# Kernel optimization log

Measured on AMD Instinct MI355X. Metric: run time of the kernel, lower is better.

## Reference

```python
import jax, jax.numpy as jnp
import numpy as np

B, S, D = 2, 4096, 1024
H, W = 16, 128
HD = D // H  # 64


def setup_inputs() -> dict:
    key = jax.random.key(0)
    ks = jax.random.split(key, 6)
    x = jax.random.normal(ks[0], (B, S, D), dtype=jnp.float32)
    # standard RoPE angle table: theta[pos, i] = pos / 10000^(2i/hd)
    inv_freq = 1.0 / (10000.0 ** (jnp.arange(0, HD, 2, dtype=jnp.float32) / HD))  # (hd/2,)
    rope_freqs = jnp.arange(S, dtype=jnp.float32)[:, None] * inv_freq[None, :]     # (S, hd/2)
    scale = 0.02
    wq = jax.random.normal(ks[1], (D, D), dtype=jnp.float32) * scale
    wk = jax.random.normal(ks[2], (D, D), dtype=jnp.float32) * scale
    wv = jax.random.normal(ks[3], (D, D), dtype=jnp.float32) * scale
    wo = jax.random.normal(ks[4], (D, D), dtype=jnp.float32) * scale
    return {"x": x, "rope_freqs": rope_freqs, "wq": wq, "wk": wk, "wv": wv, "wo": wo}


def reference(x, rope_freqs, wq, wk, wv, wo):
    Bsz, Sl, Dm = x.shape
    hd = Dm // H
    q = (x @ wq.T).reshape(Bsz, Sl, H, hd)
    k = (x @ wk.T).reshape(Bsz, Sl, H, hd)
    v = (x @ wv.T).reshape(Bsz, Sl, H, hd)

    # rotate-half RoPE, angles broadcast over batch and heads
    f = rope_freqs[:Sl]                               # (S, hd/2)
    cos = jnp.cos(f)[None, :, None, :]
    sin = jnp.sin(f)[None, :, None, :]

    def rope(t):
        t1, t2 = jnp.split(t, 2, axis=-1)
        return jnp.concatenate([t1 * cos - t2 * sin, t2 * cos + t1 * sin], axis=-1)

    q = rope(q)
    k = rope(k)

    # block-local sliding-window attention: window [q-left, q+right]
    Bk = W                       # block size == window size
    nb = Sl // Bk                # S assumed divisible by W
    left = W // 2
    right = W - left - 1

    pad = [(0, 0), (Bk, Bk), (0, 0), (0, 0)]
    kb = jnp.pad(k, pad).reshape(Bsz, nb + 2, Bk, H, hd)
    vb = jnp.pad(v, pad).reshape(Bsz, nb + 2, Bk, H, hd)
    # each query block attends to 3 consecutive key blocks (prev, self, next)
    k3 = jnp.concatenate([kb[:, :-2], kb[:, 1:-1], kb[:, 2:]], axis=2)  # (B,nb,3Bk,H,hd)
    v3 = jnp.concatenate([vb[:, :-2], vb[:, 1:-1], vb[:, 2:]], axis=2)
    qb = q.reshape(Bsz, nb, Bk, H, hd)

    scale = 1.0 / jnp.sqrt(jnp.asarray(hd, dtype=x.dtype))
    scores = jnp.einsum('bnqhd,bnkhd->bnhqk', qb, k3) * scale  # (B,nb,H,Bk,3Bk)

    r = jnp.arange(Bk)
    c = jnp.arange(3 * Bk)
    rel = c[None, :] - Bk - r[:, None]                  # key_pos - query_pos, (Bk,3Bk)
    win = (rel >= -left) & (rel <= right)
    blk = jnp.arange(nb)
    key_pos = blk[:, None] * Bk + c[None, :] - Bk       # (nb,3Bk) absolute key positions
    valid = (key_pos >= 0) & (key_pos < Sl)
    mask = win[None, :, :] & valid[:, None, :]          # (nb,Bk,3Bk)

    scores = jnp.where(mask[None, :, None, :, :], scores, jnp.asarray(-1e30, scores.dtype))
    probs = jax.nn.softmax(scores, axis=-1)
    out = jnp.einsum('bnhqk,bnkhd->bnqhd', probs, v3).reshape(Bsz, Sl, H * hd)
    return out @ wo.T
```

## Files before the change

### kernel.cpp

```cpp
#include <hip/hip_runtime.h>

typedef unsigned short u16;
typedef unsigned int   u32;
typedef __attribute__((ext_vector_type(4))) unsigned int u32x4;
typedef __attribute__((ext_vector_type(2))) unsigned int u32x2;
typedef __attribute__((ext_vector_type(8))) short        s16x8;
typedef __attribute__((ext_vector_type(4))) float        f32x4;
typedef __attribute__((ext_vector_type(2))) float        f32x2;

#define S_LEN 4096

typedef const __attribute__((address_space(1))) void gas_void;
typedef __attribute__((address_space(3))) void las_void;

__device__ __forceinline__ u16 f2bf(float f) {
    u32 u = __builtin_bit_cast(u32, f);
    u32 r = (u + 0x7fffu + ((u >> 16) & 1u)) >> 16;
    return (u16)r;
}

__device__ __forceinline__ float rmax16(float v) {
    v = fmaxf(v, __shfl_xor(v, 1));
    v = fmaxf(v, __shfl_xor(v, 2));
    v = fmaxf(v, __shfl_xor(v, 4));
    v = fmaxf(v, __shfl_xor(v, 8));
    return v;
}
__device__ __forceinline__ float rsum16(float v) {
    v += __shfl_xor(v, 1);
    v += __shfl_xor(v, 2);
    v += __shfl_xor(v, 4);
    v += __shfl_xor(v, 8);
    return v;
}

__global__ __launch_bounds__(256)
void prep_kernel(const float* __restrict__ x,
                 const float* __restrict__ wq, const float* __restrict__ wk,
                 const float* __restrict__ wv, const float* __restrict__ wo,
                 const float* __restrict__ freqs,
                 u16* __restrict__ xb, u16* __restrict__ wqkv, u16* __restrict__ wob,
                 float* __restrict__ tab) {
    const int bid = blockIdx.x;
    const int t   = threadIdx.x;
    if (bid < 8192) {
        const int i = bid * 256 + t;
        const f32x4 v = *(const f32x4*)(x + (size_t)i * 4);
        u32x2 o;
        o.x = (u32)f2bf(v.x) | ((u32)f2bf(v.y) << 16);
        o.y = (u32)f2bf(v.z) | ((u32)f2bf(v.w) << 16);
        *(u32x2*)(xb + (size_t)i * 4) = o;
    } else if (bid < 12288) {
        const int i   = (bid - 8192) * 256 + t;
        const int sel = i >> 18;
        const int loc = i & 262143;
        const float* src = (sel == 0) ? wq : (sel == 1) ? wk : (sel == 2) ? wv : wo;
        u16* dst = (sel < 3) ? (wqkv + (size_t)sel * 1048576) : wob;
        const f32x4 v = *(const f32x4*)(src + (size_t)loc * 4);
        u32x2 o;
        o.x = (u32)f2bf(v.x) | ((u32)f2bf(v.y) << 16);
        o.y = (u32)f2bf(v.z) | ((u32)f2bf(v.w) << 16);
        *(u32x2*)(dst + (size_t)loc * 4) = o;
    } else {
        const int i = (bid - 12288) * 256 + t;
        const float f = freqs[i];
        float sn, cs;
        sincosf(f, &sn, &cs);
        tab[i * 2]     = cs;
        tab[i * 2 + 1] = sn;
    }
}

#define VMW0() asm volatile("s_waitcnt vmcnt(0)" ::: "memory")
#define LGKM0() do { asm volatile("s_waitcnt lgkmcnt(0)" ::: "memory"); \
                     __builtin_amdgcn_sched_barrier(0); } while (0)
#define DSR0(d, a)   asm volatile("ds_read_b128 %0, %1"              : "=v"(d) : "v"(a))
#define DSR(d, a, o) asm volatile("ds_read_b128 %0, %1 offset:" #o   : "=v"(d) : "v"(a))
#define MFMA16(a, b, c) __builtin_amdgcn_mfma_f32_16x16x32_bf16(a, b, c, 0, 0, 0)
#define GL(p, d) __builtin_amdgcn_global_load_lds((gas_void*)(p), (las_void*)(d), 16, 0, 0)

#define FRAGS(P) s16x8 P##a0,P##a1,P##a2,P##a3,P##a4,P##a5,P##a6,P##a7, \
                       P##b0,P##b1,P##b2,P##b3,P##b4,P##b5,P##b6,P##b7

#define LOADTILE(P, CUR) do { \
    const u32 abase_ = ldsA + ((u32)(CUR) << 14) + arow; \
    const u32 bbase_ = ldsB + ((u32)(CUR) << 15) + brow; \
    const u32 aa0_ = abase_ + ck0, aa1_ = abase_ + ck1; \
    const u32 ba0_ = bbase_ + ck0, ba1_ = bbase_ + ck1; \
    DSR0(P##a0, aa0_); DSR(P##a1, aa0_, 2048); DSR(P##a2, aa0_, 4096); DSR(P##a3, aa0_, 6144); \
    DSR0(P##a4, aa1_); DSR(P##a5, aa1_, 2048); DSR(P##a6, aa1_, 4096); DSR(P##a7, aa1_, 6144); \
    DSR0(P##b0, ba0_); DSR(P##b1, ba0_, 2048); DSR(P##b2, ba0_, 4096); DSR(P##b3, ba0_, 6144); \
    DSR0(P##b4, ba1_); DSR(P##b5, ba1_, 2048); DSR(P##b6, ba1_, 4096); DSR(P##b7, ba1_, 6144); \
} while (0)

#define MFMA32(P) do { \
    __builtin_amdgcn_s_setprio(1); \
    acc[0][0]=MFMA16(P##a0,P##b0,acc[0][0]); acc[1][0]=MFMA16(P##a1,P##b0,acc[1][0]); \
    acc[2][0]=MFMA16(P##a2,P##b0,acc[2][0]); acc[3][0]=MFMA16(P##a3,P##b0,acc[3][0]); \
    acc[0][1]=MFMA16(P##a0,P##b1,acc[0][1]); acc[1][1]=MFMA16(P##a1,P##b1,acc[1][1]); \
    acc[2][1]=MFMA16(P##a2,P##b1,acc[2][1]); acc[3][1]=MFMA16(P##a3,P##b1,acc[3][1]); \
    acc[0][2]=MFMA16(P##a0,P##b2,acc[0][2]); acc[1][2]=MFMA16(P##a1,P##b2,acc[1][2]); \
    acc[2][2]=MFMA16(P##a2,P##b2,acc[2][2]); acc[3][2]=MFMA16(P##a3,P##b2,acc[3][2]); \
    acc[0][3]=MFMA16(P##a0,P##b3,acc[0][3]); acc[1][3]=MFMA16(P##a1,P##b3,acc[1][3]); \
    acc[2][3]=MFMA16(P##a2,P##b3,acc[2][3]); acc[3][3]=MFMA16(P##a3,P##b3,acc[3][3]); \
    acc[0][0]=MFMA16(P##a4,P##b4,acc[0][0]); acc[1][0]=MFMA16(P##a5,P##b4,acc[1][0]); \
    acc[2][0]=MFMA16(P##a6,P##b4,acc[2][0]); acc[3][0]=MFMA16(P##a7,P##b4,acc[3][0]); \
    acc[0][1]=MFMA16(P##a4,P##b5,acc[0][1]); acc[1][1]=MFMA16(P##a5,P##b5,acc[1][1]); \
    acc[2][1]=MFMA16(P##a6,P##b5,acc[2][1]); acc[3][1]=MFMA16(P##a7,P##b5,acc[3][1]); \
    acc[0][2]=MFMA16(P##a4,P##b6,acc[0][2]); acc[1][2]=MFMA16(P##a5,P##b6,acc[1][2]); \
    acc[2][2]=MFMA16(P##a6,P##b6,acc[2][2]); acc[3][2]=MFMA16(P##a7,P##b6,acc[3][2]); \
    acc[0][3]=MFMA16(P##a4,P##b7,acc[0][3]); acc[1][3]=MFMA16(P##a5,P##b7,acc[1][3]); \
    acc[2][3]=MFMA16(P##a6,P##b7,acc[2][3]); acc[3][3]=MFMA16(P##a7,P##b7,acc[3][3]); \
    __builtin_amdgcn_s_setprio(0); \
} while (0)

template<int MODE>
__global__ __launch_bounds__(512, 2)
void gemm_bt(const u16* __restrict__ A, const u16* __restrict__ Bw,
             void* __restrict__ Cv, const float* __restrict__ cstab) {
    __shared__ __align__(16) u16 As[2][8192];
    __shared__ __align__(16) u16 Bs[2][16384];
    const int t    = threadIdx.x;
    const int bm   = blockIdx.x << 7;
    const int bn   = blockIdx.y << 8;
    const int wave = t >> 6;
    const int wr   = (wave >> 2) & 1;
    const int wc   = wave & 3;
    const int lane = t & 63;
    const int fr   = lane & 15;
    const int kg   = lane >> 4;
    const int f7   = fr & 7;
    const int wq16 = wave << 9;
    const int K    = 1024;

    const int srow = t >> 3;
    const int cSw  = (t & 7) ^ (srow & 7);

    const u16* ga0 = A  + (size_t)(bm + srow) * K + (cSw << 3);
    const u16* ga1 = ga0 + (size_t)64 * K;
    const u16* gb0 = Bw + (size_t)(bn + srow) * K + (cSw << 3);
    const u16* gb1 = gb0 + (size_t)64 * K;
    const u16* gb2 = gb1 + (size_t)64 * K;
    const u16* gb3 = gb2 + (size_t)64 * K;

    f32x4 acc[4][4];
#pragma unroll
    for (int m = 0; m < 4; ++m)
#pragma unroll
        for (int n = 0; n < 4; ++n) acc[m][n] = f32x4{0.f, 0.f, 0.f, 0.f};

    FRAGS(X);
    FRAGS(Y);

#define STAGE(cur) do { \
    GL(ga0, &As[cur][wq16]);          GL(ga1, &As[cur][4096 + wq16]); \
    GL(gb0, &Bs[cur][wq16]);          GL(gb1, &Bs[cur][4096 + wq16]); \
    GL(gb2, &Bs[cur][8192 + wq16]);   GL(gb3, &Bs[cur][12288 + wq16]); \
    ga0 += 64; ga1 += 64; gb0 += 64; gb1 += 64; gb2 += 64; gb3 += 64; \
} while (0)

    const u32 ldsA = (u32)(size_t)(las_void*)&As[0][0];
    const u32 ldsB = (u32)(size_t)(las_void*)&Bs[0][0];
    const u32 arow = (u32)(((wr << 6) + fr) << 7);
    const u32 brow = (u32)(((wc << 6) + fr) << 7);
    const u32 ck0  = (u32)((kg ^ f7) << 4);
    const u32 ck1  = (u32)(((4 + kg) ^ f7) << 4);

    STAGE(0);
    VMW0();
    __builtin_amdgcn_s_barrier();
    LOADTILE(X, 0);
    STAGE(1);

#pragma unroll 1
    for (int j = 0; j < 16; j += 2) {
        LGKM0();
        VMW0();
        __builtin_amdgcn_s_barrier();
        if (j < 14) STAGE(0);
        LOADTILE(Y, 1);
        MFMA32(X);
        LGKM0();
        if (j < 14) {
            VMW0();
            __builtin_amdgcn_s_barrier();
            if (j < 13) STAGE(1);
            LOADTILE(X, 0);
        }
        MFMA32(Y);
    }

#undef STAGE

    if constexpr (MODE == 1) {
        const int sel   = bn >> 10;
        const int bcol  = (bn & 1023) + (wc << 6) + fr;
        const int crow0 = bm + (wr << 6) + (kg << 2);
        if (sel == 2) {
            u16* vt = (u16*)Cv + (size_t)16777216;
#pragma unroll
            for (int m = 0; m < 4; ++m) {
                const int row0 = crow0 + (m << 4);
                const int bb   = row0 >> 12;
                const int s0   = row0 & 4095;
#pragma unroll
                for (int n = 0; n < 4; ++n) {
                    u32x2 pk;
                    pk.x = (u32)f2bf(acc[m][n][0]) | ((u32)f2bf(acc[m][n][1]) << 16);
                    pk.y = (u32)f2bf(acc[m][n][2]) | ((u32)f2bf(acc[m][n][3]) << 16);
                    *(u32x2*)(vt + ((size_t)((bb << 10) + bcol + (n << 4))) * 4096 + s0) = pk;
                }
            }
        } else {
            u16* outb = (u16*)Cv + (size_t)sel * 8388608;
            const int hh = bcol >> 6;
            const int dd = bcol & 63;
#pragma unroll
            for (int m = 0; m < 4; ++m)
#pragma unroll
                for (int r = 0; r < 4; ++r) {
                    const int row = crow0 + (m << 4) + r;
                    float v0 = acc[m][0][r], v1 = acc[m][1][r], v2 = acc[m][2][r], v3 = acc[m][3][r];
                    const int s = row & (S_LEN - 1);
                    const f32x2 c0 = *(const f32x2*)(cstab + (((s << 5) + fr) << 1));
                    const f32x2 c1 = *(const f32x2*)(cstab + (((s << 5) + 16 + fr) << 1));
                    const float n0 = v0 * c0.x - v2 * c0.y;
                    const float n2 = v2 * c0.x + v0 * c0.y;
                    const float n1 = v1 * c1.x - v3 * c1.y;
                    const float n3 = v3 * c1.x + v1 * c1.y;
                    const int bb = row >> 12;
                    u16* op = outb + (((size_t)((bb << 4) + hh)) * 4096 + s) * 64 + dd;
                    op[0]  = f2bf(n0);
                    op[16] = f2bf(n1);
                    op[32] = f2bf(n2);
                    op[48] = f2bf(n3);
                }
        }
    } else {
        float* outf     = (float*)Cv;
        const int bcol  = bn + (wc << 6) + fr;
        const int crow0 = bm + (wr << 6) + (kg << 2);
#pragma unroll
        for (int m = 0; m < 4; ++m)
#pragma unroll
            for (int r = 0; r < 4; ++r) {
                const int row = crow0 + (m << 4) + r;
                float* op = outf + (size_t)row * 1024 + bcol;
                op[0]  = acc[m][0][r];
                op[16] = acc[m][1][r];
                op[32] = acc[m][2][r];
                op[48] = acc[m][3][r];
            }
    }
}

__global__ __launch_bounds__(256)
void attn_kernel(const u16* __restrict__ Q, const u16* __restrict__ K,
                 const u16* __restrict__ Vt, u16* __restrict__ O) {
    __shared__ __align__(16) u16 Ks[192 * 64];
    __shared__ __align__(16) u16 Vs[64 * 192];
    const int bid0 = blockIdx.x;
    const int bid  = ((bid0 & 7) << 8) | (bid0 >> 3);
    const int ch  = bid & 63;
    const int h   = (bid >> 6) & 15;
    const int b   = bid >> 10;
    const int qs  = ch << 6;
    const int t   = threadIdx.x;
    const int ub  = t & 192;

    const u16* kwin = K + ((size_t)((b << 4) + h) << 18);

#pragma unroll
    for (int i = 0; i < 6; ++i) {
        const int cid = (i << 8) + t;
        const int row = cid >> 3;
        const int g   = (cid & 7) ^ (row & 7);
        const int kp  = qs - 64 + row;
        const u16* src = kwin + (long)kp * 64 + (g << 3);
        GL(src, &Ks[((i << 8) + ub) << 3]);
    }
#pragma unroll
    for (int i = 0; i < 6; ++i) {
        const int cid = (i << 8) + t;
        const int d   = cid / 24;
        const int c   = cid - d * 24;
        int g = c - (d & 7) * 3;
        if (g < 0) g += 24;
        const int key = qs - 64 + (g << 3);
        const u16* src = Vt + ((size_t)((b << 10) + (h << 6) + d)) * 4096 + key;
        GL(src, &Vs[((i << 8) + ub) << 3]);
    }

    const int w    = t >> 6;
    const int lane = t & 63;
    const int fr   = lane & 15;
    const int kg   = lane >> 4;
    const int f7   = fr & 7;

    const size_t qgoff = (((size_t)((b << 4) + h)) * 4096 + qs + (w << 4) + fr) * 64 + (kg << 3);
    const s16x8 qa0 = *(const s16x8*)(Q + qgoff);
    const s16x8 qa1 = *(const s16x8*)(Q + qgoff + 32);

    VMW0();
    __syncthreads();

    f32x4 sfr[9];
#pragma unroll
    for (int n = 0; n < 9; ++n) {
        const int row = (w << 4) + (n << 4) + fr;
        f32x4 a = f32x4{0.f, 0.f, 0.f, 0.f};
        const s16x8 kb0 = *(const s16x8*)(&Ks[(row << 6) + ((kg ^ f7) << 3)]);
        const s16x8 kb1 = *(const s16x8*)(&Ks[(row << 6) + (((4 + kg) ^ f7) << 3)]);
        a = MFMA16(qa0, kb0, a);
        a = MFMA16(qa1, kb1, a);
        sfr[n] = a;
    }

    const float NEG = -__builtin_inff();
    float mx[4] = {NEG, NEG, NEG, NEG};
#pragma unroll
    for (int n = 0; n < 9; ++n) {
        const int j = (n << 4) + fr;
#pragma unroll
        for (int r = 0; r < 4; ++r) {
            const int q  = (kg << 2) + r;
            const int kp = qs - 64 + (w << 4) + j;
            const bool valid = (j >= q) && (j - q < 128) && (kp >= 0) && (kp < S_LEN);
            const float s = valid ? sfr[n][r] * 0.125f : NEG;
            sfr[n][r] = s;
            mx[r] = fmaxf(mx[r], s);
        }
    }
#pragma unroll
    for (int r = 0; r < 4; ++r) mx[r] = rmax16(mx[r]);
    float ls[4] = {0.f, 0.f, 0.f, 0.f};
#pragma unroll
    for (int n = 0; n < 9; ++n)
#pragma unroll
        for (int r = 0; r < 4; ++r) {
            const float p = __expf(sfr[n][r] - mx[r]);
            sfr[n][r] = p;
            ls[r] += p;
        }
#pragma unroll
    for (int r = 0; r < 4; ++r) ls[r] = rsum16(ls[r]);

    __syncthreads();
    u16* Pw = Ks + w * 3072;
#pragma unroll
    for (int n = 0; n < 9; ++n) {
        const int j = (n << 4) + fr;
#pragma unroll
        for (int r = 0; r < 4; ++r) {
            const int q = (kg << 2) + r;
            Pw[q * 192 + (((j >> 3) ^ (q & 7)) << 3) + (j & 7)] = f2bf(sfr[n][r]);
        }
    }
    {
        const int j = 144 + fr;
#pragma unroll
        for (int r = 0; r < 4; ++r) {
            const int q = (kg << 2) + r;
            Pw[q * 192 + (((j >> 3) ^ (q & 7)) << 3) + (j & 7)] = 0;
        }
    }
    __syncthreads();

    f32x4 o[4];
#pragma unroll
    for (int nf = 0; nf < 4; ++nf) o[nf] = f32x4{0.f, 0.f, 0.f, 0.f};
    const int cs0 = f7 * 3;
#pragma unroll
    for (int ks = 0; ks < 5; ++ks) {
        const s16x8 pa = *(const s16x8*)(&Pw[fr * 192 + ((((ks << 2) + kg) ^ f7) << 3)]);
        int c = (w << 1) + (ks << 2) + kg;
        if (c > 23) c = 23;
        int cs = c + cs0;
        if (cs >= 24) cs -= 24;
#pragma unroll
        for (int nf = 0; nf < 4; ++nf) {
            const int d = (nf << 4) + fr;
            const s16x8 vbf = *(const s16x8*)(&Vs[d * 192 + (cs << 3)]);
            o[nf] = MFMA16(pa, vbf, o[nf]);
        }
    }

    const size_t obase = ((size_t)((b << 12) + qs + (w << 4) + (kg << 2))) * 1024 + (h << 6) + fr;
#pragma unroll
    for (int r = 0; r < 4; ++r) {
        const float inv = 1.f / ls[r];
#pragma unroll
        for (int nf = 0; nf < 4; ++nf)
            O[obase + (size_t)r * 1024 + (nf << 4)] = f2bf(o[nf][r] * inv);
    }
}

extern "C" void kernel_launch(void* const* d_in, const int* in_sizes, int n_in,
                              void* d_out, int out_size, void* d_ws, size_t ws_size,
                              hipStream_t stream) {
    const float* x  = (const float*)d_in[0];
    const float* fr = (const float*)d_in[1];
    const float* wq = (const float*)d_in[2];
    const float* wk = (const float*)d_in[3];
    const float* wv = (const float*)d_in[4];
    const float* wo = (const float*)d_in[5];

    u16* ws    = (u16*)d_ws;
    u16* xb    = ws;
    u16* wqkvb = xb + 8388608;
    u16* wob   = wqkvb + 3145728;
    u16* qb    = wob + 1048576;
    u16* kb    = qb + 8388608;
    u16* vtb   = kb + 8388608;
    float* cstab = (float*)(vtb + 8388608);
    u16* ob    = xb;

    prep_kernel<<<12800, 256, 0, stream>>>(x, wq, wk, wv, wo, fr, xb, wqkvb, wob, cstab);

    dim3 gqkv(64, 12);
    gemm_bt<1><<<gqkv, 512, 0, stream>>>(xb, wqkvb, qb, cstab);

    attn_kernel<<<2048, 256, 0, stream>>>(qb, kb, vtb, ob);

    dim3 gout(64, 4);
    gemm_bt<2><<<gout, 512, 0, stream>>>(ob, wob, d_out, nullptr);
}
```

Before: 115.7 us.

## Replace QKV GEMM with 4-wave, 64x128-per-wave kernel using finer-grained K pipeline

Adds a dedicated QKV projection kernel that uses 256 threads (4 waves), each computing a 64x128 sub-tile, with a K-step of 32 and double-buffered global-to-LDS loads. Loads are split into halves and interleaved with partial MFMA groups using vmcnt-based waits. The old templated GEMM is kept only for the output projection. The aim is higher MFMA density per wave and better overlap of loads with compute, at the cost of more accumulator registers per thread and more barriers per K-step.

```diff
diff --git a/kernel.cpp b/kernel.cpp
--- a/kernel.cpp
+++ b/kernel.cpp
@@ -71,6 +71,7 @@
     }
 }
 
+#define VMW(n) asm volatile("s_waitcnt vmcnt(" #n ")" ::: "memory")
 #define VMW0() asm volatile("s_waitcnt vmcnt(0)" ::: "memory")
 #define LGKM0() do { asm volatile("s_waitcnt lgkmcnt(0)" ::: "memory"); \
                      __builtin_amdgcn_sched_barrier(0); } while (0)
@@ -78,6 +79,153 @@
 #define DSR(d, a, o) asm volatile("ds_read_b128 %0, %1 offset:" #o   : "=v"(d) : "v"(a))
 #define MFMA16(a, b, c) __builtin_amdgcn_mfma_f32_16x16x32_bf16(a, b, c, 0, 0, 0)
 #define GL(p, d) __builtin_amdgcn_global_load_lds((gas_void*)(p), (las_void*)(d), 16, 0, 0)
+
+__global__ __launch_bounds__(256, 2)
+void gemm_qkv(const u16* __restrict__ A, const u16* __restrict__ Bw,
+              void* __restrict__ Cv, const float* __restrict__ cstab) {
+    __shared__ __align__(16) u16 As[2][4096];
+    __shared__ __align__(16) u16 Bs[2][8192];
+    const int t    = threadIdx.x;
+    const int bm   = blockIdx.x << 7;
+    const int bn   = blockIdx.y << 8;
+    const int wave = t >> 6;
+    const int wr   = (wave >> 1) & 1;
+    const int wc   = wave & 1;
+    const int lane = t & 63;
+    const int fr   = lane & 15;
+    const int kg   = lane >> 4;
+    const int wq16 = wave << 9;
+    const int K    = 1024;
+
+    const int srow = t >> 2;
+    const int cg   = (t & 3) ^ ((srow >> 1) & 3);
+
+    const u16* ga0 = A  + (size_t)(bm + srow) * K + (cg << 3);
+    const u16* ga1 = ga0 + (size_t)64 * K;
+    const u16* gb0 = Bw + (size_t)(bn + srow) * K + (cg << 3);
+    const u16* gb1 = gb0 + (size_t)64 * K;
+    const u16* gb2 = gb0 + (size_t)128 * K;
+    const u16* gb3 = gb0 + (size_t)192 * K;
+
+    f32x4 acc[4][8];
+#pragma unroll
+    for (int m = 0; m < 4; ++m)
+#pragma unroll
+        for (int n = 0; n < 8; ++n) acc[m][n] = f32x4{0.f, 0.f, 0.f, 0.f};
+    s16x8 af0, af1, af2, af3, bf0, bf1, bf2, bf3;
+
+#define SGA(S)   do { GL(ga0, &As[S][wq16]); GL(ga1, &As[S][2048 + wq16]); } while (0)
+#define SGB13(S) do { GL(gb0, &Bs[S][wq16]); GL(gb2, &Bs[S][4096 + wq16]); } while (0)
+#define SGB24(S) do { GL(gb1, &Bs[S][2048 + wq16]); GL(gb3, &Bs[S][6144 + wq16]); \
+    ga0 += 32; ga1 += 32; gb0 += 32; gb1 += 32; gb2 += 32; gb3 += 32; } while (0)
+
+#define MF16(NB) do { \
+    acc[0][NB+0]=MFMA16(af0,bf0,acc[0][NB+0]); acc[1][NB+0]=MFMA16(af1,bf0,acc[1][NB+0]); \
+    acc[2][NB+0]=MFMA16(af2,bf0,acc[2][NB+0]); acc[3][NB+0]=MFMA16(af3,bf0,acc[3][NB+0]); \
+    acc[0][NB+1]=MFMA16(af0,bf1,acc[0][NB+1]); acc[1][NB+1]=MFMA16(af1,bf1,acc[1][NB+1]); \
+    acc[2][NB+1]=MFMA16(af2,bf1,acc[2][NB+1]); acc[3][NB+1]=MFMA16(af3,bf1,acc[3][NB+1]); \
+    acc[0][NB+2]=MFMA16(af0,bf2,acc[0][NB+2]); acc[1][NB+2]=MFMA16(af1,bf2,acc[1][NB+2]); \
+    acc[2][NB+2]=MFMA16(af2,bf2,acc[2][NB+2]); acc[3][NB+2]=MFMA16(af3,bf2,acc[3][NB+2]); \
+    acc[0][NB+3]=MFMA16(af0,bf3,acc[0][NB+3]); acc[1][NB+3]=MFMA16(af1,bf3,acc[1][NB+3]); \
+    acc[2][NB+3]=MFMA16(af2,bf3,acc[2][NB+3]); acc[3][NB+3]=MFMA16(af3,bf3,acc[3][NB+3]); \
+} while (0)
+
+    const u32 ldsA = (u32)(size_t)(las_void*)&As[0][0];
+    const u32 ldsB = (u32)(size_t)(las_void*)&Bs[0][0];
+    const u32 ckq  = (u32)((kg ^ ((fr >> 1) & 3)) << 4);
+    const u32 aRow = (u32)(((wr << 6) + fr) << 6) + ckq;
+    const u32 bRow = (u32)(((wc << 7) + fr) << 6) + ckq;
+
+#define QT(CUR, STG, SON) do { \
+    const u32 aB = ldsA + (CUR) * 8192u + aRow; \
+    const u32 bB = ldsB + (CUR) * 16384u + bRow; \
+    DSR0(af0, aB); DSR(af1, aB, 1024); DSR(af2, aB, 2048); DSR(af3, aB, 3072); \
+    DSR0(bf0, bB); DSR(bf1, bB, 1024); DSR(bf2, bB, 2048); DSR(bf3, bB, 3072); \
+    if (SON) { SGA(STG); SGB13(STG); } \
+    __builtin_amdgcn_s_barrier(); \
+    LGKM0(); \
+    __builtin_amdgcn_s_setprio(1); MF16(0); __builtin_amdgcn_s_setprio(0); \
+    if (SON) VMW(4); else VMW0(); \
+    __builtin_amdgcn_s_barrier(); \
+    DSR(bf0, bB, 4096); DSR(bf1, bB, 5120); DSR(bf2, bB, 6144); DSR(bf3, bB, 7168); \
+    if (SON) SGB24(STG); \
+    __builtin_amdgcn_s_barrier(); \
+    LGKM0(); \
+    __builtin_amdgcn_s_setprio(1); MF16(4); __builtin_amdgcn_s_setprio(0); \
+    if (SON) VMW(2); \
+    __builtin_amdgcn_s_barrier(); \
+} while (0)
+
+    SGA(0); SGB13(0); SGB24(0);
+    VMW(2);
+    __builtin_amdgcn_s_barrier();
+
+#pragma unroll 1
+    for (int jj = 0; jj < 15; ++jj) {
+        QT(0, 1, 1);
+        QT(1, 0, 1);
+    }
+    QT(0, 1, 1);
+    QT(1, 0, 0);
+
+#undef QT
+#undef SGA
+#undef SGB13
+#undef SGB24
+#undef MF16
+
+    const int sel   = bn >> 10;
+    const int bcol  = (bn & 1023) + (wc << 7);
+    const int crow0 = bm + (wr << 6) + (kg << 2);
+    if (sel == 2) {
+        u16* vt = (u16*)Cv + (size_t)16777216;
+#pragma unroll
+        for (int m = 0; m < 4; ++m) {
+            const int row0 = crow0 + (m << 4);
+            const int bb   = row0 >> 12;
+            const int s0   = row0 & 4095;
+#pragma unroll
+            for (int nf = 0; nf < 8; ++nf) {
+                const int col = bcol + (nf << 4) + fr;
+                const int hh  = col >> 6;
+                const int d   = col & 63;
+                u32x2 pk;
+                pk.x = (u32)f2bf(acc[m][nf][0]) | ((u32)f2bf(acc[m][nf][1]) << 16);
+                pk.y = (u32)f2bf(acc[m][nf][2]) | ((u32)f2bf(acc[m][nf][3]) << 16);
+                *(u32x2*)(vt + ((size_t)((bb << 4) + hh) * 64 + d) * 4096 + s0) = pk;
+            }
+        }
+    } else {
+        u16* outb = (u16*)Cv + (size_t)sel * 8388608;
+        const int hb = bcol >> 6;
+#pragma unroll
+        for (int m = 0; m < 4; ++m)
+#pragma unroll
+            for (int r = 0; r < 4; ++r) {
+                const int row = crow0 + (m << 4) + r;
+                const int s   = row & 4095;
+                const int bb  = row >> 12;
+                const f32x2 c0 = *(const f32x2*)(cstab + (((s << 5) + fr) << 1));
+                const f32x2 c1 = *(const f32x2*)(cstab + (((s << 5) + 16 + fr) << 1));
+#pragma unroll
+                for (int g = 0; g < 2; ++g) {
+                    u16* qp = outb + ((size_t)((bb << 4) + hb + g) * 4096 + s) * 64;
+                    {
+                        const float lo = acc[m][(g << 2) + 0][r];
+                        const float hi = acc[m][(g << 2) + 2][r];
+                        qp[fr]      = f2bf(lo * c0.x - hi * c0.y);
+                        qp[32 + fr] = f2bf(hi * c0.x + lo * c0.y);
+                    }
+                    {
+                        const float lo = acc[m][(g << 2) + 1][r];
+                        const float hi = acc[m][(g << 2) + 3][r];
+                        qp[16 + fr] = f2bf(lo * c1.x - hi * c1.y);
+                        qp[48 + fr] = f2bf(hi * c1.x + lo * c1.y);
+                    }
+                }
+            }
+    }
+}
 
 #define FRAGS(P) s16x8 P##a0,P##a1,P##a2,P##a3,P##a4,P##a5,P##a6,P##a7, \
                        P##b0,P##b1,P##b2,P##b3,P##b4,P##b5,P##b6,P##b7
@@ -114,10 +262,9 @@
     __builtin_amdgcn_s_setprio(0); \
 } while (0)
 
-template<int MODE>
 __global__ __launch_bounds__(512, 2)
-void gemm_bt(const u16* __restrict__ A, const u16* __restrict__ Bw,
-             void* __restrict__ Cv, const float* __restrict__ cstab) {
+void gemm_out(const u16* __restrict__ A, const u16* __restrict__ Bw,
+              float* __restrict__ Cv) {
     __shared__ __align__(16) u16 As[2][8192];
     __shared__ __align__(16) u16 Bs[2][16384];
     const int t    = threadIdx.x;
@@ -189,69 +336,21 @@
         }
         MFMA32(Y);
     }
-
 #undef STAGE
 
-    if constexpr (MODE == 1) {
-        const int sel   = bn >> 10;
-        const int bcol  = (bn & 1023) + (wc << 6) + fr;
-        const int crow0 = bm + (wr << 6) + (kg << 2);
-        if (sel == 2) {
-            u16* vt = (u16*)Cv + (size_t)16777216;
-#pragma unroll
-            for (int m = 0; m < 4; ++m) {
-                const int row0 = crow0 + (m << 4);
-                const int bb   = row0 >> 12;
-                const int s0   = row0 & 4095;
-#pragma unroll
-                for (int n = 0; n < 4; ++n) {
-                    u32x2 pk;
-                    pk.x = (u32)f2bf(acc[m][n][0]) | ((u32)f2bf(acc[m][n][1]) << 16);
-                    pk.y = (u32)f2bf(acc[m][n][2]) | ((u32)f2bf(acc[m][n][3]) << 16);
-                    *(u32x2*)(vt + ((size_t)((bb << 10) + bcol + (n << 4))) * 4096 + s0) = pk;
-                }
-            }
-        } else {
-            u16* outb = (u16*)Cv + (size_t)sel * 8388608;
-            const int hh = bcol >> 6;
-            const int dd = bcol & 63;
-#pragma unroll
-            for (int m = 0; m < 4; ++m)
-#pragma unroll
-                for (int r = 0; r < 4; ++r) {
-                    const int row = crow0 + (m << 4) + r;
-                    float v0 = acc[m][0][r], v1 = acc[m][1][r], v2 = acc[m][2][r], v3 = acc[m][3][r];
-                    const int s = row & (S_LEN - 1);
-                    const f32x2 c0 = *(const f32x2*)(cstab + (((s << 5) + fr) << 1));
-                    const f32x2 c1 = *(const f32x2*)(cstab + (((s << 5) + 16 + fr) << 1));
-                    const float n0 = v0 * c0.x - v2 * c0.y;
-                    const float n2 = v2 * c0.x + v0 * c0.y;
-                    const float n1 = v1 * c1.x - v3 * c1.y;
-                    const float n3 = v3 * c1.x + v1 * c1.y;
-                    const int bb = row >> 12;
-                    u16* op = outb + (((size_t)((bb << 4) + hh)) * 4096 + s) * 64 + dd;
-                    op[0]  = f2bf(n0);
-                    op[16] = f2bf(n1);
-                    op[32] = f2bf(n2);
-                    op[48] = f2bf(n3);
-                }
-        }
-    } else {
-        float* outf     = (float*)Cv;
-        const int bcol  = bn + (wc << 6) + fr;
-        const int crow0 = bm + (wr << 6) + (kg << 2);
-#pragma unroll
-        for (int m = 0; m < 4; ++m)
-#pragma unroll
-            for (int r = 0; r < 4; ++r) {
-                const int row = crow0 + (m << 4) + r;
-                float* op = outf + (size_t)row * 1024 + bcol;
-                op[0]  = acc[m][0][r];
-                op[16] = acc[m][1][r];
-                op[32] = acc[m][2][r];
-                op[48] = acc[m][3][r];
-            }
-    }
+    const int bcol  = bn + (wc << 6) + fr;
+    const int crow0 = bm + (wr << 6) + (kg << 2);
+#pragma unroll
+    for (int m = 0; m < 4; ++m)
+#pragma unroll
+        for (int r = 0; r < 4; ++r) {
+            const int row = crow0 + (m << 4) + r;
+            float* op = Cv + (size_t)row * 1024 + bcol;
+            op[0]  = acc[m][0][r];
+            op[16] = acc[m][1][r];
+            op[32] = acc[m][2][r];
+            op[48] = acc[m][3][r];
+        }
 }
 
 __global__ __launch_bounds__(256)
@@ -418,10 +517,10 @@
     prep_kernel<<<12800, 256, 0, stream>>>(x, wq, wk, wv, wo, fr, xb, wqkvb, wob, cstab);
 
     dim3 gqkv(64, 12);
-    gemm_bt<1><<<gqkv, 512, 0, stream>>>(xb, wqkvb, qb, cstab);
+    gemm_qkv<<<gqkv, 256, 0, stream>>>(xb, wqkvb, qb, cstab);
 
     attn_kernel<<<2048, 256, 0, stream>>>(qb, kb, vtb, ob);
 
     dim3 gout(64, 4);
-    gemm_bt<2><<<gout, 512, 0, stream>>>(ob, wob, d_out, nullptr);
-}
+    gemm_out<<<gout, 512, 0, stream>>>(ob, wob, (float*)d_out);
+}
```

After: 115.7 us. Within noise of the previous version (-0.0%).

## Pre-pack GEMM operands into MFMA fragment layout and load directly to registers

Applied to the files above, without the earlier changes.

The prep kernel now converts x and the weights to bf16 and writes them in an MFMA-fragment-packed layout through an LDS transpose. The attention kernel writes its output in the same packed layout. The GEMMs drop LDS staging and barriers, load fragments straight from global memory into registers with a two-tile register double buffer, and use 256 threads with a 4x8 accumulator per wave. This removes LDS traffic and block-wide synchronisation in the GEMM main loop. In exchange it raises register pressure, relies on global-memory latency hiding with no shared reuse across waves, and adds LDS work to the prep kernel.

```diff
diff --git a/kernel.cpp b/kernel.cpp
--- a/kernel.cpp
+++ b/kernel.cpp
@@ -2,6 +2,7 @@
 
 typedef unsigned short u16;
 typedef unsigned int   u32;
+typedef unsigned long long u64;
 typedef __attribute__((ext_vector_type(4))) unsigned int u32x4;
 typedef __attribute__((ext_vector_type(2))) unsigned int u32x2;
 typedef __attribute__((ext_vector_type(8))) short        s16x8;
@@ -34,67 +35,72 @@
     return v;
 }
 
+#define VMW0() asm volatile("s_waitcnt vmcnt(0)" ::: "memory")
+#define VMWS(n) do { asm volatile("s_waitcnt vmcnt(" #n ")" ::: "memory"); \
+                     __builtin_amdgcn_sched_barrier(0); } while (0)
+#define SB0() __builtin_amdgcn_sched_barrier(0)
+#define MFMA16(a, b, c) __builtin_amdgcn_mfma_f32_16x16x32_bf16(a, b, c, 0, 0, 0)
+#define GL(p, d) __builtin_amdgcn_global_load_lds((gas_void*)(p), (las_void*)(d), 16, 0, 0)
+#define GLB(d, a, o) asm volatile("global_load_dwordx4 %0, %1, off offset:" #o : "=v"(d) : "v"(a))
+
 __global__ __launch_bounds__(256)
 void prep_kernel(const float* __restrict__ x,
                  const float* __restrict__ wq, const float* __restrict__ wk,
                  const float* __restrict__ wv, const float* __restrict__ wo,
                  const float* __restrict__ freqs,
-                 u16* __restrict__ xb, u16* __restrict__ wqkv, u16* __restrict__ wob,
+                 u16* __restrict__ apk, u16* __restrict__ bpk, u16* __restrict__ wopk,
                  float* __restrict__ tab) {
     const int bid = blockIdx.x;
     const int t   = threadIdx.x;
-    if (bid < 8192) {
-        const int i = bid * 256 + t;
-        const f32x4 v = *(const f32x4*)(x + (size_t)i * 4);
-        u32x2 o;
-        o.x = (u32)f2bf(v.x) | ((u32)f2bf(v.y) << 16);
-        o.y = (u32)f2bf(v.z) | ((u32)f2bf(v.w) << 16);
-        *(u32x2*)(xb + (size_t)i * 4) = o;
-    } else if (bid < 12288) {
-        const int i   = (bid - 8192) * 256 + t;
-        const int sel = i >> 18;
-        const int loc = i & 262143;
-        const float* src = (sel == 0) ? wq : (sel == 1) ? wk : (sel == 2) ? wv : wo;
-        u16* dst = (sel < 3) ? (wqkv + (size_t)sel * 1048576) : wob;
-        const f32x4 v = *(const f32x4*)(src + (size_t)loc * 4);
-        u32x2 o;
-        o.x = (u32)f2bf(v.x) | ((u32)f2bf(v.y) << 16);
-        o.y = (u32)f2bf(v.z) | ((u32)f2bf(v.w) << 16);
-        *(u32x2*)(dst + (size_t)loc * 4) = o;
-    } else {
-        const int i = (bid - 12288) * 256 + t;
+    if (bid >= 768) {
+        const int i = (bid - 768) * 256 + t;
         const float f = freqs[i];
         float sn, cs;
         sincosf(f, &sn, &cs);
         tab[i * 2]     = cs;
         tab[i * 2 + 1] = sn;
-    }
-}
-
-#define VMW0() asm volatile("s_waitcnt vmcnt(0)" ::: "memory")
-#define LGKM0() do { asm volatile("s_waitcnt lgkmcnt(0)" ::: "memory"); \
-                     __builtin_amdgcn_sched_barrier(0); } while (0)
-#define DSR0(d, a)   asm volatile("ds_read_b128 %0, %1"              : "=v"(d) : "v"(a))
-#define DSR(d, a, o) asm volatile("ds_read_b128 %0, %1 offset:" #o   : "=v"(d) : "v"(a))
-#define MFMA16(a, b, c) __builtin_amdgcn_mfma_f32_16x16x32_bf16(a, b, c, 0, 0, 0)
-#define GL(p, d) __builtin_amdgcn_global_load_lds((gas_void*)(p), (las_void*)(d), 16, 0, 0)
-
-#define FRAGS(P) s16x8 P##a0,P##a1,P##a2,P##a3,P##a4,P##a5,P##a6,P##a7, \
+        return;
+    }
+    __shared__ u16 L[16][1032];
+    const float* src;
+    u16* dst;
+    int nft, frag0, rowblk;
+    if (bid < 512) { src = x; dst = apk; nft = 512; rowblk = bid; frag0 = bid; }
+    else {
+        const int wsel = (bid - 512) >> 6;
+        rowblk = (bid - 512) & 63;
+        src = (wsel == 0) ? wq : (wsel == 1) ? wk : (wsel == 2) ? wv : wo;
+        if (wsel < 3) { dst = bpk;  nft = 192; frag0 = wsel * 64 + rowblk; }
+        else          { dst = wopk; nft = 64;  frag0 = rowblk; }
+    }
+#pragma unroll
+    for (int r = 0; r < 16; ++r) {
+        const f32x4 v = *(const f32x4*)(src + ((size_t)(rowblk * 16 + r)) * 1024 + t * 4);
+        u16* Lp = &L[r][t * 4];
+        Lp[0] = f2bf(v.x); Lp[1] = f2bf(v.y); Lp[2] = f2bf(v.z); Lp[3] = f2bf(v.w);
+    }
+    __syncthreads();
+#pragma unroll
+    for (int i = 0; i < 8; ++i) {
+        const int idx = (i << 8) + t;
+        const int c32 = idx >> 6;
+        const int l   = idx & 63;
+        const u32x4 d = *(const u32x4*)(&L[l & 15][(c32 << 5) + ((l >> 4) << 3)]);
+        *(u32x4*)(dst + (((size_t)c32 * nft + frag0) * 64 + l) * 8) = d;
+    }
+}
+
+#define FRAGS(P) s16x8 P##a0,P##a1,P##a2,P##a3, \
                        P##b0,P##b1,P##b2,P##b3,P##b4,P##b5,P##b6,P##b7
 
-#define LOADTILE(P, CUR) do { \
-    const u32 abase_ = ldsA + ((u32)(CUR) << 14) + arow; \
-    const u32 bbase_ = ldsB + ((u32)(CUR) << 15) + brow; \
-    const u32 aa0_ = abase_ + ck0, aa1_ = abase_ + ck1; \
-    const u32 ba0_ = bbase_ + ck0, ba1_ = bbase_ + ck1; \
-    DSR0(P##a0, aa0_); DSR(P##a1, aa0_, 2048); DSR(P##a2, aa0_, 4096); DSR(P##a3, aa0_, 6144); \
-    DSR0(P##a4, aa1_); DSR(P##a5, aa1_, 2048); DSR(P##a6, aa1_, 4096); DSR(P##a7, aa1_, 6144); \
-    DSR0(P##b0, ba0_); DSR(P##b1, ba0_, 2048); DSR(P##b2, ba0_, 4096); DSR(P##b3, ba0_, 6144); \
-    DSR0(P##b4, ba1_); DSR(P##b5, ba1_, 2048); DSR(P##b6, ba1_, 4096); DSR(P##b7, ba1_, 6144); \
+#define LD_TILE(P) do { \
+    GLB(P##a0, aA, 0); GLB(P##a1, aA, 1024); GLB(P##a2, aA, 2048); GLB(P##a3, aA, 3072); \
+    GLB(P##b0, aB0, 0); GLB(P##b1, aB0, 1024); GLB(P##b2, aB0, 2048); GLB(P##b3, aB0, 3072); \
+    GLB(P##b4, aB1, 0); GLB(P##b5, aB1, 1024); GLB(P##b6, aB1, 2048); GLB(P##b7, aB1, 3072); \
+    aA += 524288u; aB0 += (u64)SBK; aB1 += (u64)SBK; \
 } while (0)
 
-#define MFMA32(P) do { \
-    __builtin_amdgcn_s_setprio(1); \
+#define MFMA32P(P) do { \
     acc[0][0]=MFMA16(P##a0,P##b0,acc[0][0]); acc[1][0]=MFMA16(P##a1,P##b0,acc[1][0]); \
     acc[2][0]=MFMA16(P##a2,P##b0,acc[2][0]); acc[3][0]=MFMA16(P##a3,P##b0,acc[3][0]); \
     acc[0][1]=MFMA16(P##a0,P##b1,acc[0][1]); acc[1][1]=MFMA16(P##a1,P##b1,acc[1][1]); \
@@ -103,98 +109,66 @@
     acc[2][2]=MFMA16(P##a2,P##b2,acc[2][2]); acc[3][2]=MFMA16(P##a3,P##b2,acc[3][2]); \
     acc[0][3]=MFMA16(P##a0,P##b3,acc[0][3]); acc[1][3]=MFMA16(P##a1,P##b3,acc[1][3]); \
     acc[2][3]=MFMA16(P##a2,P##b3,acc[2][3]); acc[3][3]=MFMA16(P##a3,P##b3,acc[3][3]); \
-    acc[0][0]=MFMA16(P##a4,P##b4,acc[0][0]); acc[1][0]=MFMA16(P##a5,P##b4,acc[1][0]); \
-    acc[2][0]=MFMA16(P##a6,P##b4,acc[2][0]); acc[3][0]=MFMA16(P##a7,P##b4,acc[3][0]); \
-    acc[0][1]=MFMA16(P##a4,P##b5,acc[0][1]); acc[1][1]=MFMA16(P##a5,P##b5,acc[1][1]); \
-    acc[2][1]=MFMA16(P##a6,P##b5,acc[2][1]); acc[3][1]=MFMA16(P##a7,P##b5,acc[3][1]); \
-    acc[0][2]=MFMA16(P##a4,P##b6,acc[0][2]); acc[1][2]=MFMA16(P##a5,P##b6,acc[1][2]); \
-    acc[2][2]=MFMA16(P##a6,P##b6,acc[2][2]); acc[3][2]=MFMA16(P##a7,P##b6,acc[3][2]); \
-    acc[0][3]=MFMA16(P##a4,P##b7,acc[0][3]); acc[1][3]=MFMA16(P##a5,P##b7,acc[1][3]); \
-    acc[2][3]=MFMA16(P##a6,P##b7,acc[2][3]); acc[3][3]=MFMA16(P##a7,P##b7,acc[3][3]); \
-    __builtin_amdgcn_s_setprio(0); \
+    acc[0][4]=MFMA16(P##a0,P##b4,acc[0][4]); acc[1][4]=MFMA16(P##a1,P##b4,acc[1][4]); \
+    acc[2][4]=MFMA16(P##a2,P##b4,acc[2][4]); acc[3][4]=MFMA16(P##a3,P##b4,acc[3][4]); \
+    acc[0][5]=MFMA16(P##a0,P##b5,acc[0][5]); acc[1][5]=MFMA16(P##a1,P##b5,acc[1][5]); \
+    acc[2][5]=MFMA16(P##a2,P##b5,acc[2][5]); acc[3][5]=MFMA16(P##a3,P##b5,acc[3][5]); \
+    acc[0][6]=MFMA16(P##a0,P##b6,acc[0][6]); acc[1][6]=MFMA16(P##a1,P##b6,acc[1][6]); \
+    acc[2][6]=MFMA16(P##a2,P##b6,acc[2][6]); acc[3][6]=MFMA16(P##a3,P##b6,acc[3][6]); \
+    acc[0][7]=MFMA16(P##a0,P##b7,acc[0][7]); acc[1][7]=MFMA16(P##a1,P##b7,acc[1][7]); \
+    acc[2][7]=MFMA16(P##a2,P##b7,acc[2][7]); acc[3][7]=MFMA16(P##a3,P##b7,acc[3][7]); \
 } while (0)
 
-template<int MODE>
-__global__ __launch_bounds__(512, 2)
-void gemm_bt(const u16* __restrict__ A, const u16* __restrict__ Bw,
+template<int SBK, int MODE>
+__global__ __launch_bounds__(256, 2)
+void gemm_pk(const u16* __restrict__ Apk, const u16* __restrict__ Bpk,
              void* __restrict__ Cv, const float* __restrict__ cstab) {
-    __shared__ __align__(16) u16 As[2][8192];
-    __shared__ __align__(16) u16 Bs[2][16384];
     const int t    = threadIdx.x;
     const int bm   = blockIdx.x << 7;
     const int bn   = blockIdx.y << 8;
     const int wave = t >> 6;
-    const int wr   = (wave >> 2) & 1;
-    const int wc   = wave & 3;
+    const int wr   = (wave >> 1) & 1;
+    const int wc   = wave & 1;
     const int lane = t & 63;
     const int fr   = lane & 15;
     const int kg   = lane >> 4;
-    const int f7   = fr & 7;
-    const int wq16 = wave << 9;
-    const int K    = 1024;
-
-    const int srow = t >> 3;
-    const int cSw  = (t & 7) ^ (srow & 7);
-
-    const u16* ga0 = A  + (size_t)(bm + srow) * K + (cSw << 3);
-    const u16* ga1 = ga0 + (size_t)64 * K;
-    const u16* gb0 = Bw + (size_t)(bn + srow) * K + (cSw << 3);
-    const u16* gb1 = gb0 + (size_t)64 * K;
-    const u16* gb2 = gb1 + (size_t)64 * K;
-    const u16* gb3 = gb2 + (size_t)64 * K;
-
-    f32x4 acc[4][4];
+
+    u64 aA  = (u64)(uintptr_t)Apk + (u64)(((bm >> 4) + (wr << 2)) * 1024 + lane * 16);
+    u64 aB0 = (u64)(uintptr_t)Bpk + (u64)(((bn >> 4) + (wc << 3)) * 1024 + lane * 16);
+    u64 aB1 = aB0 + 4096u;
+
+    f32x4 acc[4][8];
 #pragma unroll
     for (int m = 0; m < 4; ++m)
 #pragma unroll
-        for (int n = 0; n < 4; ++n) acc[m][n] = f32x4{0.f, 0.f, 0.f, 0.f};
+        for (int n = 0; n < 8; ++n) acc[m][n] = f32x4{0.f, 0.f, 0.f, 0.f};
 
     FRAGS(X);
     FRAGS(Y);
 
-#define STAGE(cur) do { \
-    GL(ga0, &As[cur][wq16]);          GL(ga1, &As[cur][4096 + wq16]); \
-    GL(gb0, &Bs[cur][wq16]);          GL(gb1, &Bs[cur][4096 + wq16]); \
-    GL(gb2, &Bs[cur][8192 + wq16]);   GL(gb3, &Bs[cur][12288 + wq16]); \
-    ga0 += 64; ga1 += 64; gb0 += 64; gb1 += 64; gb2 += 64; gb3 += 64; \
-} while (0)
-
-    const u32 ldsA = (u32)(size_t)(las_void*)&As[0][0];
-    const u32 ldsB = (u32)(size_t)(las_void*)&Bs[0][0];
-    const u32 arow = (u32)(((wr << 6) + fr) << 7);
-    const u32 brow = (u32)(((wc << 6) + fr) << 7);
-    const u32 ck0  = (u32)((kg ^ f7) << 4);
-    const u32 ck1  = (u32)(((4 + kg) ^ f7) << 4);
-
-    STAGE(0);
+    LD_TILE(X);
+    LD_TILE(Y);
+
+#pragma unroll 1
+    for (int i = 0; i < 15; ++i) {
+        VMWS(12);
+        MFMA32P(X);
+        SB0();
+        LD_TILE(X);
+        VMWS(12);
+        MFMA32P(Y);
+        SB0();
+        LD_TILE(Y);
+    }
+    VMWS(12);
+    MFMA32P(X);
     VMW0();
-    __builtin_amdgcn_s_barrier();
-    LOADTILE(X, 0);
-    STAGE(1);
-
-#pragma unroll 1
-    for (int j = 0; j < 16; j += 2) {
-        LGKM0();
-        VMW0();
-        __builtin_amdgcn_s_barrier();
-        if (j < 14) STAGE(0);
-        LOADTILE(Y, 1);
-        MFMA32(X);
-        LGKM0();
-        if (j < 14) {
-            VMW0();
-            __builtin_amdgcn_s_barrier();
-            if (j < 13) STAGE(1);
-            LOADTILE(X, 0);
-        }
-        MFMA32(Y);
-    }
-
-#undef STAGE
+    SB0();
+    MFMA32P(Y);
 
     if constexpr (MODE == 1) {
         const int sel   = bn >> 10;
-        const int bcol  = (bn & 1023) + (wc << 6) + fr;
+        const int bcol  = (bn & 1023) + (wc << 7);
         const int crow0 = bm + (wr << 6) + (kg << 2);
         if (sel == 2) {
             u16* vt = (u16*)Cv + (size_t)16777216;
@@ -204,41 +178,49 @@
                 const int bb   = row0 >> 12;
                 const int s0   = row0 & 4095;
 #pragma unroll
-                for (int n = 0; n < 4; ++n) {
+                for (int nf = 0; nf < 8; ++nf) {
+                    const int col = bcol + (nf << 4) + fr;
+                    const int hh  = col >> 6;
+                    const int d   = col & 63;
                     u32x2 pk;
-                    pk.x = (u32)f2bf(acc[m][n][0]) | ((u32)f2bf(acc[m][n][1]) << 16);
-                    pk.y = (u32)f2bf(acc[m][n][2]) | ((u32)f2bf(acc[m][n][3]) << 16);
-                    *(u32x2*)(vt + ((size_t)((bb << 10) + bcol + (n << 4))) * 4096 + s0) = pk;
+                    pk.x = (u32)f2bf(acc[m][nf][0]) | ((u32)f2bf(acc[m][nf][1]) << 16);
+                    pk.y = (u32)f2bf(acc[m][nf][2]) | ((u32)f2bf(acc[m][nf][3]) << 16);
+                    *(u32x2*)(vt + ((size_t)((bb << 4) + hh) * 64 + d) * 4096 + s0) = pk;
                 }
             }
         } else {
             u16* outb = (u16*)Cv + (size_t)sel * 8388608;
-            const int hh = bcol >> 6;
-            const int dd = bcol & 63;
+            const int hb = bcol >> 6;
 #pragma unroll
             for (int m = 0; m < 4; ++m)
 #pragma unroll
                 for (int r = 0; r < 4; ++r) {
                     const int row = crow0 + (m << 4) + r;
-                    float v0 = acc[m][0][r], v1 = acc[m][1][r], v2 = acc[m][2][r], v3 = acc[m][3][r];
-                    const int s = row & (S_LEN - 1);
+                    const int s   = row & 4095;
+                    const int bb  = row >> 12;
                     const f32x2 c0 = *(const f32x2*)(cstab + (((s << 5) + fr) << 1));
                     const f32x2 c1 = *(const f32x2*)(cstab + (((s << 5) + 16 + fr) << 1));
-                    const float n0 = v0 * c0.x - v2 * c0.y;
-                    const float n2 = v2 * c0.x + v0 * c0.y;
-                    const float n1 = v1 * c1.x - v3 * c1.y;
-                    const float n3 = v3 * c1.x + v1 * c1.y;
-                    const int bb = row >> 12;
-                    u16* op = outb + (((size_t)((bb << 4) + hh)) * 4096 + s) * 64 + dd;
-                    op[0]  = f2bf(n0);
-                    op[16] = f2bf(n1);
-                    op[32] = f2bf(n2);
-                    op[48] = f2bf(n3);
+#pragma unroll
+                    for (int g = 0; g < 2; ++g) {
+                        u16* qp = outb + ((size_t)((bb << 4) + hb + g) * 4096 + s) * 64;
+                        {
+                            const float lo = acc[m][(g << 2) + 0][r];
+                            const float hi = acc[m][(g << 2) + 2][r];
+                            qp[fr]      = f2bf(lo * c0.x - hi * c0.y);
+                            qp[32 + fr] = f2bf(hi * c0.x + lo * c0.y);
+                        }
+                        {
+                            const float lo = acc[m][(g << 2) + 1][r];
+                            const float hi = acc[m][(g << 2) + 3][r];
+                            qp[16 + fr] = f2bf(lo * c1.x - hi * c1.y);
+                            qp[48 + fr] = f2bf(hi * c1.x + lo * c1.y);
+                        }
+                    }
                 }
         }
     } else {
         float* outf     = (float*)Cv;
-        const int bcol  = bn + (wc << 6) + fr;
+        const int bcol  = bn + (wc << 7) + fr;
         const int crow0 = bm + (wr << 6) + (kg << 2);
 #pragma unroll
         for (int m = 0; m < 4; ++m)
@@ -246,10 +228,9 @@
             for (int r = 0; r < 4; ++r) {
                 const int row = crow0 + (m << 4) + r;
                 float* op = outf + (size_t)row * 1024 + bcol;
-                op[0]  = acc[m][0][r];
-                op[16] = acc[m][1][r];
-                op[32] = acc[m][2][r];
-                op[48] = acc[m][3][r];
+#pragma unroll
+                for (int nf = 0; nf < 8; ++nf)
+                    op[nf << 4] = acc[m][nf][r];
             }
     }
 }
@@ -385,13 +366,17 @@
         }
     }
 
-    const size_t obase = ((size_t)((b << 12) + qs + (w << 4) + (kg << 2))) * 1024 + (h << 6) + fr;
+    const int mfrag = (b << 8) + (ch << 2) + w;
 #pragma unroll
     for (int r = 0; r < 4; ++r) {
         const float inv = 1.f / ls[r];
 #pragma unroll
-        for (int nf = 0; nf < 4; ++nf)
-            O[obase + (size_t)r * 1024 + (nf << 4)] = f2bf(o[nf][r] * inv);
+        for (int nf = 0; nf < 4; ++nf) {
+            const int kt  = (h << 1) + (nf >> 1);
+            const int kgp = ((nf & 1) << 1) + (fr >> 3);
+            const int lp  = (kgp << 4) + (kg << 2) + r;
+            O[((((size_t)kt << 9) + mfrag) * 64 + lp) * 8 + (fr & 7)] = f2bf(o[nf][r] * inv);
+        }
     }
 }
 
@@ -406,22 +391,22 @@
     const float* wo = (const float*)d_in[5];
 
     u16* ws    = (u16*)d_ws;
-    u16* xb    = ws;
-    u16* wqkvb = xb + 8388608;
-    u16* wob   = wqkvb + 3145728;
-    u16* qb    = wob + 1048576;
+    u16* apk   = ws;
+    u16* bpk   = apk + 8388608;
+    u16* wopk  = bpk + 3145728;
+    u16* qb    = wopk + 1048576;
     u16* kb    = qb + 8388608;
     u16* vtb   = kb + 8388608;
     float* cstab = (float*)(vtb + 8388608);
-    u16* ob    = xb;
-
-    prep_kernel<<<12800, 256, 0, stream>>>(x, wq, wk, wv, wo, fr, xb, wqkvb, wob, cstab);
+    u16* opk   = apk;
+
+    prep_kernel<<<1280, 256, 0, stream>>>(x, wq, wk, wv, wo, fr, apk, bpk, wopk, cstab);
 
     dim3 gqkv(64, 12);
-    gemm_bt<1><<<gqkv, 512, 0, stream>>>(xb, wqkvb, qb, cstab);
-
-    attn_kernel<<<2048, 256, 0, stream>>>(qb, kb, vtb, ob);
+    gemm_pk<196608, 1><<<gqkv, 256, 0, stream>>>(apk, bpk, qb, cstab);
+
+    attn_kernel<<<2048, 256, 0, stream>>>(qb, kb, vtb, opk);
 
     dim3 gout(64, 4);
-    gemm_bt<2><<<gout, 512, 0, stream>>>(ob, wob, d_out, nullptr);
-}
+    gemm_pk<65536, 2><<<gout, 256, 0, stream>>>(opk, wopk, (float*)d_out, nullptr);
+}
```

After: 109.1 us. 5.7% less time.
